# Optimization experiments

Hardware: AMD Instinct MI355X
Metric: run time of the kernel (lower is better)

## Reference

```python
import jax, jax.numpy as jnp
import numpy as np

ALPHA = 0.2  # LeakyReLU negative slope

def setup_inputs() -> dict:
    key = jax.random.key(0)
    k1, k2, k3 = jax.random.split(key, 3)
    B, N, D_in, D_out = 4, 512, 512, 256
    H = jax.random.normal(k1, (B, N, D_in), dtype=jnp.float32)
    # xavier-style scaled params
    W = jax.random.normal(k2, (D_out, D_in), dtype=jnp.float32) * (2.0 / (D_in + D_out)) ** 0.5
    a = jax.random.normal(k3, (D_out, 1), dtype=jnp.float32) * (2.0 / (D_out + 1)) ** 0.5
    return {"H": H, "W": W, "a": a}

def reference(H, W, a):
    # Wh: [B, N, D_out]
    Wh = jnp.einsum('bnd,od->bno', H, W)
    # additive pairwise scores: e[b,i,j] = leakyrelu(Wh[b,i]+Wh[b,j]) . a
    e = jnp.einsum('bijo,o->bij',
                   jax.nn.leaky_relu(Wh[:, :, None, :] + Wh[:, None, :, :], ALPHA),
                   a[:, 0])
    attention = jax.nn.softmax(e, axis=-1)          # [B, N, N]
    H_att = jnp.einsum('bij,bjo->bio', attention, Wh)  # [B, N, D_out]
    return H_att
```

## Files before the change

### kernel.cpp

```cpp
#include <hip/hip_runtime.h>

constexpr int Bq   = 4;
constexpr int Nq   = 512;
constexpr int DIN  = 512;
constexpr int DOUT = 256;

typedef _Float16 h2  __attribute__((ext_vector_type(2)));
typedef _Float16 h4  __attribute__((ext_vector_type(4)));
typedef _Float16 h8  __attribute__((ext_vector_type(8)));
typedef float    f4v __attribute__((ext_vector_type(4)));

#if defined(__has_builtin) && __has_builtin(__builtin_amdgcn_fdot2)
__device__ __forceinline__ float fdot2f(h2 a, h2 b, float c) {
    return __builtin_amdgcn_fdot2(a, b, c, false);
}
#else
__device__ __forceinline__ float fdot2f(h2 a, h2 b, float c) {
    return (float)a.x * (float)b.x + (float)a.y * (float)b.y + c;
}
#endif

__device__ __forceinline__ h8 cvt8(float4 lo, float4 hi) {
    h8 r;
    r[0] = (_Float16)lo.x; r[1] = (_Float16)lo.y;
    r[2] = (_Float16)lo.z; r[3] = (_Float16)lo.w;
    r[4] = (_Float16)hi.x; r[5] = (_Float16)hi.y;
    r[6] = (_Float16)hi.z; r[7] = (_Float16)hi.w;
    return r;
}

__global__ __launch_bounds__(256) void k1_wh(const float* __restrict__ H,
                                             const float* __restrict__ W,
                                             const float* __restrict__ a,
                                             h2* __restrict__ Wh16,
                                             h2* __restrict__ WhT16p,
                                             h2* __restrict__ WhT16n,
                                             h2* __restrict__ a16) {
    const int bid = blockIdx.x;
    const int t   = threadIdx.x;

    if (bid == 512) {
        if (t < 64) {
            const int idx = 2 * t;
            const float4 v = *(const float4*)&a[2 * idx];
            h2 h0; h0.x = (_Float16)v.x; h0.y = (_Float16)v.y;
            h2 h1; h1.x = (_Float16)v.z; h1.y = (_Float16)v.w;
            a16[idx] = h0; a16[idx + 1] = h1;
        }
        return;
    }

    const int w    = t >> 6;
    const int lane = t & 63;
    const int mt   = bid >> 2;
    const int b    = mt & 3;
    const int n0   = (mt >> 2) << 4;
    const int o0   = ((bid & 3) << 6) + (w << 4);
    const int quad = lane >> 4;
    const int col  = lane & 15;

    const float4* __restrict__ aP =
        (const float4*)(H + (size_t)(b * Nq + n0 + col) * DIN) + quad * 2;
    const float4* __restrict__ bP =
        (const float4*)(W + (size_t)(o0 + col) * DIN) + quad * 2;

    f4v acc = {0.f, 0.f, 0.f, 0.f};
    float4 fa0 = aP[0], fa1 = aP[1];
    float4 fb0 = bP[0], fb1 = bP[1];

#pragma unroll
    for (int kb = 0; kb < 16; ++kb) {
        float4 na0 = fa0, na1 = fa1, nb0 = fb0, nb1 = fb1;
        if (kb < 15) {
            na0 = aP[(kb + 1) * 8];
            na1 = aP[(kb + 1) * 8 + 1];
            nb0 = bP[(kb + 1) * 8];
            nb1 = bP[(kb + 1) * 8 + 1];
        }
        const h8 af = cvt8(fa0, fa1);
        const h8 bf = cvt8(fb0, fb1);
        acc = __builtin_amdgcn_mfma_f32_16x16x32_f16(af, bf, acc, 0, 0, 0);
        fa0 = na0; fa1 = na1; fb0 = nb0; fb1 = nb1;
    }

    const int rloc = n0 + quad * 4;

    h4 hj;
    hj[0] = (_Float16)acc[0]; hj[1] = (_Float16)acc[1];
    hj[2] = (_Float16)acc[2]; hj[3] = (_Float16)acc[3];
    *(h4*)(WhT16n + ((size_t)(b * 256 + o0 + col)) * 256 + (rloc >> 1)) = hj;

#pragma unroll
    for (int reg = 0; reg < 4; ++reg) {
        const float v  = acc[reg];
        const float vp = __shfl_xor(v, 1);
        if ((col & 1) == 0) {
            h2 hv; hv.x = (_Float16)v; hv.y = (_Float16)vp;
            const int o2 = (o0 + col) >> 1;
            Wh16[(size_t)(b * Nq + rloc + reg) * 128 + o2] = hv;
            WhT16p[(size_t)b * 65536 + (size_t)o2 * 512 + (rloc + reg)] = hv;
        }
    }
}

__global__ __launch_bounds__(1024, 8) void k23(const h2* __restrict__ Wh16,
                                               const h2* __restrict__ WhT16p,
                                               const h2* __restrict__ WhT16n,
                                               const h2* __restrict__ a16,
                                               float* __restrict__ out) {
    const int t   = threadIdx.x;
    const int blk = blockIdx.x;
    const int b   = blk & 3;
    const int i0  = (blk >> 2) << 2;

    __shared__ float smem[8192];
    __shared__ __align__(16) h2 sPh[4 * 272];
    __shared__ float wred[2][4][8];

    {
        const int h  = __builtin_amdgcn_readfirstlane(t >> 9);
        const int j  = t & 511;
        const int ob = h * 64;

        const h2* __restrict__ wjp = WhT16p + (size_t)b * 65536 + (size_t)ob * 512 + j;
        const h2* __restrict__ wip = Wh16 + (size_t)(b * Nq + i0) * 128;

        float ab[4] = {0.f, 0.f, 0.f, 0.f};
        float rja = 0.f;
        h2 cA[8], cB[8];

#define K2_L8(buf, kb)                                                      \
    _Pragma("unroll") for (int s = 0; s < 8; ++s)                           \
        buf[s] = wjp[((kb) + s) * 512];

#define K2_C8(buf, kb)                                                      \
    _Pragma("unroll") for (int s = 0; s < 8; ++s) {                         \
        const int o2 = ob + (kb) + s;                                       \
        const h2 a2 = a16[o2];                                  \
        rja = fdot2f(a2, buf[s], rja);                                      \
        _Pragma("unroll") for (int rr = 0; rr < 4; ++rr) {                  \
            const h2 wi = wip[rr * 128 + o2];                   \
            h2 w  = buf[s] + wi;                                \
            h2 aw = __builtin_elementwise_max(w, -w);           \
            ab[rr] = fdot2f(a2, aw, ab[rr]);                    \
        }                                                                   \
    }

        K2_L8(cA, 0)  K2_L8(cB, 8)
        K2_C8(cA, 0)  K2_L8(cA, 16)
        K2_C8(cB, 8)  K2_L8(cB, 24)
        K2_C8(cA, 16) K2_L8(cA, 32)
        K2_C8(cB, 24) K2_L8(cB, 40)
        K2_C8(cA, 32) K2_L8(cA, 48)
        K2_C8(cB, 40) K2_L8(cB, 56)
        K2_C8(cA, 48)
        K2_C8(cB, 56)
#undef K2_L8
#undef K2_C8

        float* sAb = smem;
        float* sRh = smem + 2048;
        float* sRf = smem + 2560;
        if (h == 1) {
#pragma unroll
            for (int rr = 0; rr < 4; ++rr) sAb[rr * 512 + j] = ab[rr];
            sRh[j] = rja;
        }
        __syncthreads();

        float rj = 0.f;
        if (h == 0) {
#pragma unroll
            for (int rr = 0; rr < 4; ++rr) ab[rr] += sAb[rr * 512 + j];
            rj = rja + sRh[j];
            sRf[j] = rj;
        }
        __syncthreads();

        float e[4], pv[4];
        const int lane = t & 63;
        const int w    = t >> 6;

        if (h == 0) {
#pragma unroll
            for (int rr = 0; rr < 4; ++rr)
                e[rr] = 0.6f * (sRf[i0 + rr] + rj) + 0.4f * ab[rr];
#pragma unroll
            for (int rr = 0; rr < 4; ++rr) {
                float v = e[rr];
#pragma unroll
                for (int off = 32; off > 0; off >>= 1) v = fmaxf(v, __shfl_xor(v, off));
                if (lane == 0) wred[0][rr][w] = v;
            }
        }
        __syncthreads();
        if (h == 0) {
#pragma unroll
            for (int rr = 0; rr < 4; ++rr) {
                const float4 q0 = *(const float4*)&wred[0][rr][0];
                const float4 q1 = *(const float4*)&wred[0][rr][4];
                const float m = fmaxf(fmaxf(fmaxf(q0.x, q0.y), fmaxf(q0.z, q0.w)),
                                      fmaxf(fmaxf(q1.x, q1.y), fmaxf(q1.z, q1.w)));
                pv[rr] = __expf(e[rr] - m);
            }
#pragma unroll
            for (int rr = 0; rr < 4; ++rr) {
                float v = pv[rr];
#pragma unroll
                for (int off = 32; off > 0; off >>= 1) v += __shfl_xor(v, off);
                if (lane == 0) wred[1][rr][w] = v;
            }
        }
        __syncthreads();
        if (h == 0) {
#pragma unroll
            for (int rr = 0; rr < 4; ++rr) {
                const float4 q0 = *(const float4*)&wred[1][rr][0];
                const float4 q1 = *(const float4*)&wred[1][rr][4];
                const float s = (q0.x + q0.y + q0.z + q0.w) + (q1.x + q1.y + q1.z + q1.w);
                const float pn = pv[rr] * (1.0f / s);
                const float pp = __shfl_xor(pn, 1);
                if ((j & 1) == 0) {
                    h2 hv; hv.x = (_Float16)pn; hv.y = (_Float16)pp;
                    sPh[rr * 272 + (j >> 1)] = hv;
                }
            }
        }
        __syncthreads();
    }

    {
        const int w16  = __builtin_amdgcn_readfirstlane(t >> 6);
        const int lane = t & 63;
        const int quad = lane >> 4;
        const int col  = lane & 15;
        const int o0   = w16 << 4;

        const h2* __restrict__ wt =
            WhT16n + (size_t)b * 65536 + (size_t)(o0 + col) * 256 + quad * 4;
        const h2* __restrict__ ap = sPh + (col & 3) * 272 + quad * 4;

        f4v acc = {0.f, 0.f, 0.f, 0.f};
        h8 b0 = *(const h8*)wt;
#pragma unroll
        for (int kb = 0; kb < 16; ++kb) {
            h8 b1 = b0;
            if (kb < 15) b1 = *(const h8*)(wt + (kb + 1) * 16);
            const h8 af = *(const h8*)(ap + kb * 16);
            acc = __builtin_amdgcn_mfma_f32_16x16x32_f16(af, b0, acc, 0, 0, 0);
            b0 = b1;
        }

        if (quad == 0) {
#pragma unroll
            for (int reg = 0; reg < 4; ++reg) {
                out[((size_t)(b * Nq) + i0 + reg) * DOUT + o0 + col] = acc[reg];
            }
        }
    }
}

extern "C" void kernel_launch(void* const* d_in, const int* in_sizes, int n_in,
                              void* d_out, int out_size, void* d_ws, size_t ws_size,
                              hipStream_t stream) {
    const float* H = (const float*)d_in[0];
    const float* W = (const float*)d_in[1];
    const float* a = (const float*)d_in[2];
    float* out = (float*)d_out;

    h2* Wh16   = (h2*)d_ws;
    h2* WhT16p = Wh16 + 262144;
    h2* WhT16n = WhT16p + 262144;
    h2* a16    = WhT16n + 262144;

    hipLaunchKernelGGL(k1_wh, dim3(513), dim3(256),  0, stream, H, W, a, Wh16, WhT16p, WhT16n, a16);
    hipLaunchKernelGGL(k23,   dim3(512), dim3(1024), 0, stream, Wh16, WhT16p, WhT16n, a16, out);
}
```

Baseline: 107.0 us.

## Split-K the Wh GEMM across waves and widen the transposed Wh layout to half4

The first kernel now uses twice as many blocks. Each pair of waves splits the K dimension in half and combines the partial MFMA results through shared memory, which raises parallelism in the projection GEMM. The transposed Wh buffer is repacked in groups of four halves, so the score kernel loads h4 instead of h2 and runs half as many load iterations with two fdot2 per element. The costs are an extra block-level sync and reduction in k1 and more shuffles when storing the packed layout.

New measurement: 106.7 us. No clear change (-0.3%).

```diff
diff --git a/kernel.cpp b/kernel.cpp
--- a/kernel.cpp
+++ b/kernel.cpp
@@ -39,7 +39,7 @@
     const int bid = blockIdx.x;
     const int t   = threadIdx.x;
 
-    if (bid == 512) {
+    if (bid == 1024) {
         if (t < 64) {
             const int idx = 2 * t;
             const float4 v = *(const float4*)&a[2 * idx];
@@ -52,26 +52,27 @@
 
     const int w    = t >> 6;
     const int lane = t & 63;
-    const int mt   = bid >> 2;
-    const int b    = mt & 3;
-    const int n0   = (mt >> 2) << 4;
-    const int o0   = ((bid & 3) << 6) + (w << 4);
+    const int T    = (bid << 1) | (w & 1);
+    const int kh   = w >> 1;
+    const int b    = (T >> 4) & 3;
+    const int n0   = (T >> 6) << 4;
+    const int o0   = (T & 15) << 4;
     const int quad = lane >> 4;
     const int col  = lane & 15;
 
     const float4* __restrict__ aP =
-        (const float4*)(H + (size_t)(b * Nq + n0 + col) * DIN) + quad * 2;
+        (const float4*)(H + (size_t)(b * Nq + n0 + col) * DIN) + kh * 64 + quad * 2;
     const float4* __restrict__ bP =
-        (const float4*)(W + (size_t)(o0 + col) * DIN) + quad * 2;
+        (const float4*)(W + (size_t)(o0 + col) * DIN) + kh * 64 + quad * 2;
 
     f4v acc = {0.f, 0.f, 0.f, 0.f};
     float4 fa0 = aP[0], fa1 = aP[1];
     float4 fb0 = bP[0], fb1 = bP[1];
 
 #pragma unroll
-    for (int kb = 0; kb < 16; ++kb) {
+    for (int kb = 0; kb < 8; ++kb) {
         float4 na0 = fa0, na1 = fa1, nb0 = fb0, nb1 = fb1;
-        if (kb < 15) {
+        if (kb < 7) {
             na0 = aP[(kb + 1) * 8];
             na1 = aP[(kb + 1) * 8 + 1];
             nb0 = bP[(kb + 1) * 8];
@@ -83,22 +84,42 @@
         fa0 = na0; fa1 = na1; fb0 = nb0; fb1 = nb1;
     }
 
-    const int rloc = n0 + quad * 4;
-
-    h4 hj;
-    hj[0] = (_Float16)acc[0]; hj[1] = (_Float16)acc[1];
-    hj[2] = (_Float16)acc[2]; hj[3] = (_Float16)acc[3];
-    *(h4*)(WhT16n + ((size_t)(b * 256 + o0 + col)) * 256 + (rloc >> 1)) = hj;
-
-#pragma unroll
-    for (int reg = 0; reg < 4; ++reg) {
-        const float v  = acc[reg];
-        const float vp = __shfl_xor(v, 1);
-        if ((col & 1) == 0) {
+    __shared__ f4v sPart[2][64];
+    if (kh) sPart[w & 1][lane] = acc;
+    __syncthreads();
+    if (!kh) {
+        const f4v p = sPart[w & 1][lane];
+#pragma unroll
+        for (int r = 0; r < 4; ++r) acc[r] += p[r];
+
+        const int rloc = n0 + quad * 4;
+
+        h4 hj;
+        hj[0] = (_Float16)acc[0]; hj[1] = (_Float16)acc[1];
+        hj[2] = (_Float16)acc[2]; hj[3] = (_Float16)acc[3];
+        *(h4*)(WhT16n + ((size_t)(b * 256 + o0 + col)) * 256 + (rloc >> 1)) = hj;
+
+        h4* __restrict__ WhT16p4 = (h4*)WhT16p;
+#pragma unroll
+        for (int reg = 0; reg < 4; ++reg) {
+            const float v  = acc[reg];
+            const float vp = __shfl_xor(v, 1);
             h2 hv; hv.x = (_Float16)v; hv.y = (_Float16)vp;
-            const int o2 = (o0 + col) >> 1;
-            Wh16[(size_t)(b * Nq + rloc + reg) * 128 + o2] = hv;
-            WhT16p[(size_t)b * 65536 + (size_t)o2 * 512 + (rloc + reg)] = hv;
+            unsigned u;
+            __builtin_memcpy(&u, &hv, 4);
+            const unsigned u2 = __shfl_xor(u, 2);
+            if ((col & 1) == 0) {
+                const int o2 = (o0 + col) >> 1;
+                Wh16[(size_t)(b * Nq + rloc + reg) * 128 + o2] = hv;
+            }
+            if ((col & 3) == 0) {
+                h2 hv2;
+                __builtin_memcpy(&hv2, &u2, 4);
+                h4 q;
+                q[0] = hv[0]; q[1] = hv[1]; q[2] = hv2[0]; q[3] = hv2[1];
+                const int o4 = (o0 + col) >> 2;
+                WhT16p4[(size_t)b * 32768 + (size_t)o4 * 512 + (rloc + reg)] = q;
+            }
         }
     }
 }
@@ -118,43 +139,49 @@
     __shared__ float wred[2][4][8];
 
     {
-        const int h  = __builtin_amdgcn_readfirstlane(t >> 9);
-        const int j  = t & 511;
-        const int ob = h * 64;
-
-        const h2* __restrict__ wjp = WhT16p + (size_t)b * 65536 + (size_t)ob * 512 + j;
-        const h2* __restrict__ wip = Wh16 + (size_t)(b * Nq + i0) * 128;
+        const int h   = __builtin_amdgcn_readfirstlane(t >> 9);
+        const int j   = t & 511;
+        const int ob4 = h * 32;
+
+        const h4* __restrict__ wjp  = (const h4*)WhT16p + (size_t)b * 32768 + j;
+        const h4* __restrict__ wip4 = (const h4*)Wh16 + (size_t)(b * Nq + i0) * 64;
+        const h4* __restrict__ a4p  = (const h4*)a16;
 
         float ab[4] = {0.f, 0.f, 0.f, 0.f};
         float rja = 0.f;
-        h2 cA[8], cB[8];
+        h4 cA[8], cB[8];
 
 #define K2_L8(buf, kb)                                                      \
     _Pragma("unroll") for (int s = 0; s < 8; ++s)                           \
-        buf[s] = wjp[((kb) + s) * 512];
+        buf[s] = wjp[((size_t)(ob4 + (kb) + s)) * 512];
 
 #define K2_C8(buf, kb)                                                      \
     _Pragma("unroll") for (int s = 0; s < 8; ++s) {                         \
-        const int o2 = ob + (kb) + s;                                       \
-        const h2 a2 = a16[o2];                                  \
-        rja = fdot2f(a2, buf[s], rja);                                      \
+        const int o4 = ob4 + (kb) + s;                                      \
+        const h4 a4 = a4p[o4];                               \
+        const h2 alo = __builtin_shufflevector(a4, a4, 0, 1);               \
+        const h2 ahi = __builtin_shufflevector(a4, a4, 2, 3);               \
+        const h4 c  = buf[s];                                               \
+        const h2 clo = __builtin_shufflevector(c, c, 0, 1);                 \
+        const h2 chi = __builtin_shufflevector(c, c, 2, 3);                 \
+        rja = fdot2f(alo, clo, rja);                                        \
+        rja = fdot2f(ahi, chi, rja);                                        \
         _Pragma("unroll") for (int rr = 0; rr < 4; ++rr) {                  \
-            const h2 wi = wip[rr * 128 + o2];                   \
-            h2 w  = buf[s] + wi;                                \
-            h2 aw = __builtin_elementwise_max(w, -w);           \
-            ab[rr] = fdot2f(a2, aw, ab[rr]);                    \
+            const h4 wi = wip4[rr * 64 + o4];                \
+            const h2 wl = clo + __builtin_shufflevector(wi, wi, 0, 1);      \
+            const h2 wh_ = chi + __builtin_shufflevector(wi, wi, 2, 3);     \
+            const h2 awl = __builtin_elementwise_max(wl, -wl);              \
+            const h2 awh = __builtin_elementwise_max(wh_, -wh_);            \
+            ab[rr] = fdot2f(alo, awl, ab[rr]);                              \
+            ab[rr] = fdot2f(ahi, awh, ab[rr]);                              \
         }                                                                   \
     }
 
         K2_L8(cA, 0)  K2_L8(cB, 8)
         K2_C8(cA, 0)  K2_L8(cA, 16)
         K2_C8(cB, 8)  K2_L8(cB, 24)
-        K2_C8(cA, 16) K2_L8(cA, 32)
-        K2_C8(cB, 24) K2_L8(cB, 40)
-        K2_C8(cA, 32) K2_L8(cA, 48)
-        K2_C8(cB, 40) K2_L8(cB, 56)
-        K2_C8(cA, 48)
-        K2_C8(cB, 56)
+        K2_C8(cA, 16)
+        K2_C8(cB, 24)
 #undef K2_L8
 #undef K2_C8
 
@@ -273,6 +300,6 @@
     h2* WhT16n = WhT16p + 262144;
     h2* a16    = WhT16n + 262144;
 
-    hipLaunchKernelGGL(k1_wh, dim3(513), dim3(256),  0, stream, H, W, a, Wh16, WhT16p, WhT16n, a16);
-    hipLaunchKernelGGL(k23,   dim3(512), dim3(1024), 0, stream, Wh16, WhT16p, WhT16n, a16, out);
-}
+    hipLaunchKernelGGL(k1_wh, dim3(1025), dim3(256),  0, stream, H, W, a, Wh16, WhT16p, WhT16n, a16);
+    hipLaunchKernelGGL(k23,   dim3(512),  dim3(1024), 0, stream, Wh16, WhT16p, WhT16n, a16, out);
+}
```
